# Kernel optimization log

Hardware: AMD Instinct MI355X
Metric: run time of the kernel (lower is better)

Reference implementation:

```python
import jax, jax.numpy as jnp
import numpy as np

GROUPS = 4
SF = 2   # scale_factor
K = 3    # filter_k

def conv1x1(x, w, b):
    return jnp.einsum('bchw,oc->bohw', x, w) + b[None, :, None, None]

def grid_sample(img, grid):
    # img: (N,C,H,W); grid: (N,Hg,Wg,2) xy in [-1,1]; bilinear, border padding, align_corners=False
    N, C, H, W = img.shape
    ix = jnp.clip(((grid[..., 0] + 1.0) * W - 1.0) * 0.5, 0.0, W - 1.0)
    iy = jnp.clip(((grid[..., 1] + 1.0) * H - 1.0) * 0.5, 0.0, H - 1.0)
    x0 = jnp.floor(ix); y0 = jnp.floor(iy)
    wx = (ix - x0)[..., None]; wy = (iy - y0)[..., None]
    x0i = x0.astype(jnp.int32); y0i = y0.astype(jnp.int32)
    x1i = jnp.minimum(x0i + 1, W - 1); y1i = jnp.minimum(y0i + 1, H - 1)
    bidx = jnp.arange(N)[:, None, None]
    v00 = img[bidx, :, y0i, x0i]; v01 = img[bidx, :, y0i, x1i]
    v10 = img[bidx, :, y1i, x0i]; v11 = img[bidx, :, y1i, x1i]   # (N,Hg,Wg,C)
    out = (v00 * (1 - wx) * (1 - wy) + v01 * wx * (1 - wy)
           + v10 * (1 - wx) * wy + v11 * wx * wy)
    return jnp.transpose(out, (0, 3, 1, 2))

def def_sample(x, off):
    b, c, h, w = x.shape
    g = GROUPS
    off = off.reshape(b * g, SF, SF, 2, h, w).transpose(0, 4, 1, 5, 2, 3)
    hd, wd = SF * h, SF * w
    off = off.reshape(b * g, hd, wd, 2)
    gy, gx = jnp.meshgrid(jnp.arange(hd, dtype=x.dtype) + 0.5,
                          jnp.arange(wd, dtype=x.dtype) + 0.5, indexing='ij')
    base = jnp.stack([gx, gy], axis=-1)[None]
    grid = 2.0 * (base + off) / jnp.array([wd, hd], dtype=x.dtype) - 1.0
    return grid_sample(x.reshape(b * g, c // g, h, w), grid).reshape(b, c, hd, wd)

def dyn_filter(x, compress, kw, kb):
    b, c, h, w = x.shape
    kern = jax.nn.softmax(conv1x1(compress, kw, kb), axis=1)  # (b,K*K,h,w)
    p = K // 2
    xp = jnp.pad(x, ((0, 0), (0, 0), (p, p), (p, p)))
    patches = jnp.stack([xp[:, :, dy:dy + h, dx:dx + w]
                         for dy in range(K) for dx in range(K)], axis=2)  # (b,c,K*K,h,w)
    return jnp.einsum('bkhw,bckhw->bchw', kern, patches)

def trim_op(x, toff):
    b, c, h, w = x.shape
    g = GROUPS
    off = toff.reshape(b, g, 2, h, w).transpose(0, 1, 3, 4, 2)  # (b,g,h,w,2) xy
    gy, gx = jnp.meshgrid(jnp.arange(h, dtype=x.dtype) + 0.5,
                          jnp.arange(w, dtype=x.dtype) + 0.5, indexing='ij')
    base = jnp.stack([gx, gy], axis=-1)[None, None]
    grid = (2.0 * (base + off) / jnp.array([w, h], dtype=x.dtype) - 1.0).reshape(b * g, h, w, 2)
    return grid_sample(x.reshape(b * g, c // g, h, w), grid).reshape(b, c, h, w)

def setup_inputs():
    key = jax.random.key(0)
    ks = jax.random.split(key, 13)
    C = 256
    oc = GROUPS * SF * SF * 2  # 32
    f = jnp.float32
    return {
        "x": jax.random.normal(ks[0], (4, C, 64, 64), f),
        "def_off_w": jax.random.normal(ks[1], (oc, C), f) * 0.001,
        "def_off_b": jnp.zeros((oc,), f),
        "def_ast_w": jax.random.normal(ks[2], (oc, C), f) * 0.01,
        "def_ast_b": jnp.zeros((oc,), f),
        "comp_w": jax.random.normal(ks[3], (64, C), f) * (1.0 / np.sqrt(C).astype(np.float32)),
        "comp_b": jnp.zeros((64,), f),
        "filt_w": jax.random.normal(ks[4], (K * K, 64), f) * 0.001,
        "filt_b": jnp.zeros((K * K,), f),
        "trim_w": jax.random.normal(ks[5], (GROUPS * 2, 64), f) * 0.001,
        "trim_b": jnp.zeros((GROUPS * 2,), f),
        "trim_ast_w": jax.random.normal(ks[6], (GROUPS * 2, 64), f) * 0.01,
        "trim_ast_b": jnp.zeros((GROUPS * 2,), f),
    }

def reference(x, def_off_w, def_off_b, def_ast_w, def_ast_b, comp_w, comp_b,
              filt_w, filt_b, trim_w, trim_b, trim_ast_w, trim_ast_b):
    off = conv1x1(x, def_off_w, def_off_b) * jax.nn.sigmoid(conv1x1(x, def_ast_w, def_ast_b))
    x_up = def_sample(x, off)                              # (b,c,2h,2w)
    comp = conv1x1(x_up, comp_w, comp_b)                   # (b,64,2h,2w)
    x_filt = dyn_filter(x_up, comp, filt_w, filt_b)
    toff = conv1x1(comp, trim_w, trim_b) * jax.nn.sigmoid(conv1x1(comp, trim_ast_w, trim_ast_b))
    return trim_op(x_filt, toff)
```

## Files before the change

kernel.cpp:

```cpp
#include <hip/hip_runtime.h>
#include <hip/hip_bf16.h>
#include <string.h>

typedef __hip_bfloat16 bf16;
typedef __attribute__((ext_vector_type(8))) short short8;
typedef __attribute__((ext_vector_type(4))) short short4v;
typedef __attribute__((ext_vector_type(4))) float f32x4;

__device__ __forceinline__ float b2f(bf16 v) { return __bfloat162float(v); }
__device__ __forceinline__ bf16  f2b(float v) { return __float2bfloat16(v); }
__device__ __forceinline__ float s2f(short s) {
    return __uint_as_float(((unsigned)(unsigned short)s) << 16);
}
__device__ __forceinline__ short f2s(float v) {
    bf16 t = f2b(v); short s; __builtin_memcpy(&s, &t, 2); return s;
}

#define CC 256
#define HWD 16384

__global__ __launch_bounds__(256) void k0_xpose(const float* __restrict__ x,
        bf16* __restrict__ xpm)
{
    __shared__ short tile[64][258];
    int b = blockIdx.x >> 6;
    int p0 = (blockIdx.x & 63) << 6;
    int lp = threadIdx.x & 63;
    int c0 = threadIdx.x >> 6;
    const float* xb = x + ((size_t)b << 20);
    for (int k = 0; k < 64; ++k) {
        int c = c0 * 64 + k;
        tile[lp][c] = f2s(xb[((size_t)c << 12) + p0 + lp]);
    }
    __syncthreads();
    int lc = threadIdx.x & 63;
    int s = threadIdx.x >> 6;
    short* ob = (short*)xpm + ((size_t)(b * 4096 + p0) << 8) + s * 64 + lc;
    for (int r = 0; r < 64; ++r)
        ob[(size_t)r << 8] = tile[r][s * 64 + lc];
}

__global__ __launch_bounds__(256) void k1_off(const bf16* __restrict__ xpm,
        const float* __restrict__ w_off, const float* __restrict__ b_off,
        const float* __restrict__ w_ast, const float* __restrict__ b_ast,
        float* __restrict__ offpm)
{
    const int b = blockIdx.x >> 6;
    const int p0 = (blockIdx.x & 63) << 6;
    const int lane = threadIdx.x & 63;
    const int n = lane & 15, quad = lane >> 4;
    const int jb = (threadIdx.x >> 6) << 4;
    const int j = jb + n, oc = j >> 1, kind = j & 1;

    short8 bfrag[8];
    const float* wrow = (kind ? w_ast : w_off) + oc * 256 + quad * 8;
#pragma unroll
    for (int kc = 0; kc < 8; ++kc) {
        float4 lo = *(const float4*)(wrow + kc * 32);
        float4 hi = *(const float4*)(wrow + kc * 32 + 4);
        short8 f;
        f[0] = f2s(lo.x); f[1] = f2s(lo.y); f[2] = f2s(lo.z); f[3] = f2s(lo.w);
        f[4] = f2s(hi.x); f[5] = f2s(hi.y); f[6] = f2s(hi.z); f[7] = f2s(hi.w);
        bfrag[kc] = f;
    }
    float bias = kind ? b_ast[oc] : b_off[oc];

    const short* abase = (const short*)xpm + ((size_t)(b * 4096) << 8);
    float* obase = offpm + ((size_t)(b * 4096) << 5);

#pragma unroll
    for (int mt = 0; mt < 4; mt += 2) {
        f32x4 acc0 = {0.f, 0.f, 0.f, 0.f};
        f32x4 acc1 = {0.f, 0.f, 0.f, 0.f};
        const short8* ar0 = (const short8*)(abase + (((size_t)(p0 + mt * 16 + n)) << 8) + quad * 8);
        const short8* ar1 = (const short8*)(abase + (((size_t)(p0 + mt * 16 + 16 + n)) << 8) + quad * 8);
#pragma unroll
        for (int kc = 0; kc < 8; ++kc) {
            short8 a0 = ar0[kc * 4];
            short8 a1 = ar1[kc * 4];
            acc0 = __builtin_amdgcn_mfma_f32_16x16x32_bf16(a0, bfrag[kc], acc0, 0, 0, 0);
            acc1 = __builtin_amdgcn_mfma_f32_16x16x32_bf16(a1, bfrag[kc], acc1, 0, 0, 0);
        }
#pragma unroll
        for (int r = 0; r < 4; ++r) {
            float v0 = acc0[r] + bias;
            float v1 = acc1[r] + bias;
            float p0v = __shfl_xor(v0, 1, 64);
            float p1v = __shfl_xor(v1, 1, 64);
            if (!(n & 1)) {
                int px = p0 + mt * 16 + quad * 4 + r;
                obase[((size_t)px << 5) + oc] = v0 * (1.f / (1.f + expf(-p0v)));
                obase[((size_t)(px + 16) << 5) + oc] = v1 * (1.f / (1.f + expf(-p1v)));
            }
        }
    }
}

__global__ __launch_bounds__(256) void k2_defsample(const bf16* __restrict__ xpm,
        const float* __restrict__ offpm, bf16* __restrict__ xup)
{
    int p = blockIdx.x * 4 + (threadIdx.x >> 6);
    int lane = threadIdx.x & 63;
    int b = p >> 14, hw = p & 16383;
    int hy = hw >> 7, wx = hw & 127;
    int h = hy >> 1, w = wx >> 1;
    int g = lane >> 4;
    int och = (g << 3) + ((hy & 1) << 2) + ((wx & 1) << 1);
    const float* orow = offpm + ((size_t)(b * 4096 + (h << 6) + w) << 5);
    float ox = orow[och], oy = orow[och + 1];
    float ix = (wx + 0.5f + ox) * 0.5f - 0.5f;
    float iy = (hy + 0.5f + oy) * 0.5f - 0.5f;
    ix = fminf(fmaxf(ix, 0.f), 63.f);
    iy = fminf(fmaxf(iy, 0.f), 63.f);
    float x0f = floorf(ix), y0f = floorf(iy);
    float fx = ix - x0f, fy = iy - y0f;
    int x0 = (int)x0f, y0 = (int)y0f;
    int x1 = min(x0 + 1, 63), y1 = min(y0 + 1, 63);
    float w00 = (1.f - fx) * (1.f - fy), w01 = fx * (1.f - fy);
    float w10 = (1.f - fx) * fy,        w11 = fx * fy;
    const short* xb = (const short*)xpm + ((size_t)b << 20);
    int e = lane * 4;
    short4v v00 = *(const short4v*)(xb + (((size_t)(y0 << 6) + x0) << 8) + e);
    short4v v01 = *(const short4v*)(xb + (((size_t)(y0 << 6) + x1) << 8) + e);
    short4v v10 = *(const short4v*)(xb + (((size_t)(y1 << 6) + x0) << 8) + e);
    short4v v11 = *(const short4v*)(xb + (((size_t)(y1 << 6) + x1) << 8) + e);
    short4v pk;
#pragma unroll
    for (int j = 0; j < 4; ++j) {
        float v = w00 * s2f(v00[j]) + w01 * s2f(v01[j])
                + w10 * s2f(v10[j]) + w11 * s2f(v11[j]);
        pk[j] = f2s(v);
    }
    *(short4v*)((short*)xup + (((size_t)(b * HWD + hw)) << 8) + e) = pk;
}

__global__ __launch_bounds__(256) void k3_fused(const bf16* __restrict__ xup,
        const float* __restrict__ cw, const float* __restrict__ cb,
        const float* __restrict__ fw_g, const float* __restrict__ fb,
        const float* __restrict__ tw, const float* __restrict__ tb,
        const float* __restrict__ taw, const float* __restrict__ tab,
        bf16* __restrict__ kern, float* __restrict__ toff)
{
    __shared__ float smc[64][65];
    __shared__ __align__(16) float fwS[64 * 12];
    __shared__ __align__(16) float swS[64 * 16];
    for (int i = threadIdx.x; i < 64 * 12; i += 256) {
        int c = i / 12, k = i % 12;
        fwS[i] = (k < 9) ? fw_g[k * 64 + c] : 0.f;
    }
    for (int i = threadIdx.x; i < 64 * 16; i += 256) {
        int c = i >> 4, jj = i & 15;
        int oc = jj >> 1, kind = jj & 1;
        swS[i] = kind ? taw[oc * 64 + c] : tw[oc * 64 + c];
    }

    const int b = blockIdx.x >> 8;
    const int hw0 = (blockIdx.x & 255) << 6;
    const int lane = threadIdx.x & 63;
    const int n = lane & 15, quad = lane >> 4;
    const int ocb = (threadIdx.x >> 6) << 4;

    short8 bfrag[8];
    const float* wrow = cw + (ocb + n) * 256 + quad * 8;
#pragma unroll
    for (int kc = 0; kc < 8; ++kc) {
        float4 lo = *(const float4*)(wrow + kc * 32);
        float4 hi = *(const float4*)(wrow + kc * 32 + 4);
        short8 f;
        f[0] = f2s(lo.x); f[1] = f2s(lo.y); f[2] = f2s(lo.z); f[3] = f2s(lo.w);
        f[4] = f2s(hi.x); f[5] = f2s(hi.y); f[6] = f2s(hi.z); f[7] = f2s(hi.w);
        bfrag[kc] = f;
    }
    float bias = cb[ocb + n];

    const short* abase = (const short*)xup + ((size_t)(b * HWD) << 8);

#pragma unroll
    for (int mt = 0; mt < 4; mt += 2) {
        f32x4 acc0 = {0.f, 0.f, 0.f, 0.f};
        f32x4 acc1 = {0.f, 0.f, 0.f, 0.f};
        const short8* ar0 = (const short8*)(abase + (((size_t)(hw0 + mt * 16 + n)) << 8) + quad * 8);
        const short8* ar1 = (const short8*)(abase + (((size_t)(hw0 + mt * 16 + 16 + n)) << 8) + quad * 8);
#pragma unroll
        for (int kc = 0; kc < 8; ++kc) {
            short8 a0 = ar0[kc * 4];
            short8 a1 = ar1[kc * 4];
            acc0 = __builtin_amdgcn_mfma_f32_16x16x32_bf16(a0, bfrag[kc], acc0, 0, 0, 0);
            acc1 = __builtin_amdgcn_mfma_f32_16x16x32_bf16(a1, bfrag[kc], acc1, 0, 0, 0);
        }
#pragma unroll
        for (int r = 0; r < 4; ++r) {
            smc[mt * 16 + quad * 4 + r][ocb + n] = acc0[r] + bias;
            smc[mt * 16 + 16 + quad * 4 + r][ocb + n] = acc1[r] + bias;
        }
    }
    __syncthreads();

    const int px = threadIdx.x & 63;
    const int q = threadIdx.x >> 6;
    const int hw = hw0 + px;
    if (q == 0) {
        float a[9];
#pragma unroll
        for (int k = 0; k < 9; ++k) a[k] = fb[k];
        for (int c = 0; c < 64; ++c) {
            float v = smc[px][c];
            const float4* wr = reinterpret_cast<const float4*>(&fwS[c * 12]);
            float4 w0 = wr[0], w1 = wr[1];
            float w8 = fwS[c * 12 + 8];
            a[0] += v * w0.x; a[1] += v * w0.y; a[2] += v * w0.z; a[3] += v * w0.w;
            a[4] += v * w1.x; a[5] += v * w1.y; a[6] += v * w1.z; a[7] += v * w1.w;
            a[8] += v * w8;
        }
        float mx = a[0];
#pragma unroll
        for (int k = 1; k < 9; ++k) mx = fmaxf(mx, a[k]);
        float s = 0.f;
#pragma unroll
        for (int k = 0; k < 9; ++k) { a[k] = expf(a[k] - mx); s += a[k]; }
        float inv = 1.f / s;
        short* kr = (short*)kern + ((size_t)(b * HWD + hw) << 4);
        short8 pk;
#pragma unroll
        for (int k = 0; k < 8; ++k) pk[k] = f2s(a[k] * inv);
        *(short8*)kr = pk;
        kr[8] = f2s(a[8] * inv);
    } else {
        const int oc0 = (q == 3) ? 6 : (q - 1) * 3;
        const int noc = (q == 3) ? 2 : 3;
        float o[3], aa[3];
        for (int i = 0; i < noc; ++i) { o[i] = tb[oc0 + i]; aa[i] = tab[oc0 + i]; }
        for (int c = 0; c < 64; ++c) {
            float v = smc[px][c];
            const float* wr = &swS[c << 4];
#pragma unroll 3
            for (int i = 0; i < noc; ++i) {
                o[i]  += v * wr[2 * (oc0 + i)];
                aa[i] += v * wr[2 * (oc0 + i) + 1];
            }
        }
        for (int i = 0; i < noc; ++i)
            toff[((size_t)(b * 8 + oc0 + i) << 14) + hw] =
                o[i] * (1.f / (1.f + expf(-aa[i])));
    }
}

__global__ __launch_bounds__(256) void k4b_apply(const bf16* __restrict__ xup,
        const bf16* __restrict__ kern, bf16* __restrict__ xfilt)
{
    int t = blockIdx.x * 256 + threadIdx.x;
    int chunk = t & 31;
    int hw = (t >> 5) & 16383;
    int b = t >> 19;
    int h = hw >> 7, w = hw & 127;

    const short* kr = (const short*)kern + ((size_t)(b * HWD + hw) << 4);
    short8 k8 = *(const short8*)kr;
    float wk[9];
#pragma unroll
    for (int k = 0; k < 8; ++k) wk[k] = s2f(k8[k]);
    wk[8] = s2f(kr[8]);

    float ymask[3] = { h > 0 ? 1.f : 0.f, 1.f, h < 127 ? 1.f : 0.f };
    float xmask[3] = { w > 0 ? 1.f : 0.f, 1.f, w < 127 ? 1.f : 0.f };
    int hy[3] = { (max(h - 1, 0)) << 7, h << 7, (min(h + 1, 127)) << 7 };
    int wx[3] = { max(w - 1, 0), w, min(w + 1, 127) };

    const short* xb = (const short*)xup + ((size_t)(b * HWD) << 8) + chunk * 8;
    float sum[8];
#pragma unroll
    for (int j = 0; j < 8; ++j) sum[j] = 0.f;
#pragma unroll
    for (int dy = 0; dy < 3; ++dy) {
#pragma unroll
        for (int dx = 0; dx < 3; ++dx) {
            float wgt = wk[dy * 3 + dx] * ymask[dy] * xmask[dx];
            short8 v = *(const short8*)(xb + ((size_t)(hy[dy] + wx[dx]) << 8));
#pragma unroll
            for (int j = 0; j < 8; ++j) sum[j] += wgt * s2f(v[j]);
        }
    }
    short8 pk;
#pragma unroll
    for (int j = 0; j < 8; ++j) pk[j] = f2s(sum[j]);
    *(short8*)((short*)xfilt + ((size_t)(b * HWD + hw) << 8) + chunk * 8) = pk;
}

__global__ __launch_bounds__(256) void k6_trim(const bf16* __restrict__ xfilt,
        const float* __restrict__ toff, float* __restrict__ out)
{
    __shared__ float sm[32][260];
    int b = blockIdx.x >> 9;
    int hw0 = (blockIdx.x & 511) << 5;
    int wave = threadIdx.x >> 6, lane = threadIdx.x & 63;
    int e = lane * 4;
    int g = lane >> 4;
    const short* xb = (const short*)xfilt + ((size_t)(b * HWD) << 8);
    const float* tfx = toff + ((size_t)(b * 8 + 2 * g)     << 14);
    const float* tfy = toff + ((size_t)(b * 8 + 2 * g + 1) << 14);

    for (int i = 0; i < 8; ++i) {
        int pp = wave * 8 + i;
        int hw = hw0 + pp;
        int h = hw >> 7, w = hw & 127;
        float ox = tfx[hw], oy = tfy[hw];
        float ix = fminf(fmaxf(w + ox, 0.f), 127.f);
        float iy = fminf(fmaxf(h + oy, 0.f), 127.f);
        float x0f = floorf(ix), y0f = floorf(iy);
        float fx = ix - x0f, fy = iy - y0f;
        int x0 = (int)x0f, y0 = (int)y0f;
        int x1 = min(x0 + 1, 127), y1 = min(y0 + 1, 127);
        float w00 = (1.f - fx) * (1.f - fy), w01 = fx * (1.f - fy);
        float w10 = (1.f - fx) * fy,        w11 = fx * fy;
        short4v v00 = *(const short4v*)(xb + (((size_t)(y0 << 7) + x0) << 8) + e);
        short4v v01 = *(const short4v*)(xb + (((size_t)(y0 << 7) + x1) << 8) + e);
        short4v v10 = *(const short4v*)(xb + (((size_t)(y1 << 7) + x0) << 8) + e);
        short4v v11 = *(const short4v*)(xb + (((size_t)(y1 << 7) + x1) << 8) + e);
#pragma unroll
        for (int j = 0; j < 4; ++j) {
            sm[pp][e + j] = w00 * s2f(v00[j]) + w01 * s2f(v01[j])
                          + w10 * s2f(v10[j]) + w11 * s2f(v11[j]);
        }
    }
    __syncthreads();
    int lp = threadIdx.x & 31;
    int c0 = (threadIdx.x >> 5) << 5;
    float* ob = out + (((size_t)b << 8) << 14) + hw0 + lp;
#pragma unroll 8
    for (int k = 0; k < 32; ++k) {
        int c = c0 + k;
        ob[(size_t)c << 14] = sm[lp][c];
    }
}

extern "C" void kernel_launch(void* const* d_in, const int* in_sizes, int n_in,
                              void* d_out, int out_size, void* d_ws, size_t ws_size,
                              hipStream_t stream)
{
    const float* x       = (const float*)d_in[0];
    const float* w_off   = (const float*)d_in[1];
    const float* b_off   = (const float*)d_in[2];
    const float* w_ast   = (const float*)d_in[3];
    const float* b_ast   = (const float*)d_in[4];
    const float* comp_w  = (const float*)d_in[5];
    const float* comp_b  = (const float*)d_in[6];
    const float* filt_w  = (const float*)d_in[7];
    const float* filt_b  = (const float*)d_in[8];
    const float* trim_w  = (const float*)d_in[9];
    const float* trim_b  = (const float*)d_in[10];
    const float* trim_aw = (const float*)d_in[11];
    const float* trim_ab = (const float*)d_in[12];
    float* out = (float*)d_out;

    char* ws = (char*)d_ws;
    float* offpm = (float*)(ws);
    bf16*  kern  = (bf16*) (ws);
    bf16*  xup   = (bf16*) (ws + (2ull << 20));
    bf16*  xpm   = (bf16*) (ws + (34ull << 20));
    bf16*  xfilt = (bf16*) (ws + (50ull << 20));
    float* toff  = (float*)(ws + (82ull << 20));

    hipLaunchKernelGGL(k0_xpose,    dim3(256),   dim3(256), 0, stream,
                       x, xpm);
    hipLaunchKernelGGL(k1_off,      dim3(256),   dim3(256), 0, stream,
                       xpm, w_off, b_off, w_ast, b_ast, offpm);
    hipLaunchKernelGGL(k2_defsample,dim3(16384), dim3(256), 0, stream,
                       xpm, offpm, xup);
    hipLaunchKernelGGL(k3_fused,    dim3(1024),  dim3(256), 0, stream,
                       xup, comp_w, comp_b, filt_w, filt_b,
                       trim_w, trim_b, trim_aw, trim_ab, kern, toff);
    hipLaunchKernelGGL(k4b_apply,   dim3(8192),  dim3(256), 0, stream,
                       xup, kern, xfilt);
    hipLaunchKernelGGL(k6_trim,     dim3(2048),  dim3(256), 0, stream,
                       xfilt, toff, out);
}
```

Baseline: 190.9 us.

## Fuse transpose with offset conv and deformable sampling with compress conv

Merges the transpose kernel into the offset conv kernel so the transposed tile stays in swizzled shared memory and feeds the MFMA directly. It also merges deformable sampling into the compress-conv kernel, so the upsampled tile is built in LDS and used for the GEMM without being read back from global memory. The xup buffer is still written for the later filter kernel, and kern moves to its own workspace region because it no longer aliases offpm. Two launches and one global re-read are removed, at the cost of larger shared-memory use and lower occupancy in the fused kernels.

```diff
diff --git a/kernel.cpp b/kernel.cpp
--- a/kernel.cpp
+++ b/kernel.cpp
@@ -19,39 +19,20 @@
 #define CC 256
 #define HWD 16384
 
-__global__ __launch_bounds__(256) void k0_xpose(const float* __restrict__ x,
-        bf16* __restrict__ xpm)
-{
-    __shared__ short tile[64][258];
-    int b = blockIdx.x >> 6;
-    int p0 = (blockIdx.x & 63) << 6;
-    int lp = threadIdx.x & 63;
-    int c0 = threadIdx.x >> 6;
-    const float* xb = x + ((size_t)b << 20);
-    for (int k = 0; k < 64; ++k) {
-        int c = c0 * 64 + k;
-        tile[lp][c] = f2s(xb[((size_t)c << 12) + p0 + lp]);
-    }
-    __syncthreads();
-    int lc = threadIdx.x & 63;
-    int s = threadIdx.x >> 6;
-    short* ob = (short*)xpm + ((size_t)(b * 4096 + p0) << 8) + s * 64 + lc;
-    for (int r = 0; r < 64; ++r)
-        ob[(size_t)r << 8] = tile[r][s * 64 + lc];
-}
-
-__global__ __launch_bounds__(256) void k1_off(const bf16* __restrict__ xpm,
+__global__ __launch_bounds__(256) void k01_xpose_off(const float* __restrict__ x,
         const float* __restrict__ w_off, const float* __restrict__ b_off,
         const float* __restrict__ w_ast, const float* __restrict__ b_ast,
-        float* __restrict__ offpm)
-{
+        bf16* __restrict__ xpm, float* __restrict__ offpm)
+{
+    __shared__ __align__(16) short tileS[64 * 256];
     const int b = blockIdx.x >> 6;
     const int p0 = (blockIdx.x & 63) << 6;
     const int lane = threadIdx.x & 63;
+    const int wave = threadIdx.x >> 6;
     const int n = lane & 15, quad = lane >> 4;
-    const int jb = (threadIdx.x >> 6) << 4;
+
+    const int jb = wave << 4;
     const int j = jb + n, oc = j >> 1, kind = j & 1;
-
     short8 bfrag[8];
     const float* wrow = (kind ? w_ast : w_off) + oc * 256 + quad * 8;
 #pragma unroll
@@ -65,19 +46,44 @@
     }
     float bias = kind ? b_ast[oc] : b_off[oc];
 
-    const short* abase = (const short*)xpm + ((size_t)(b * 4096) << 8);
-    float* obase = offpm + ((size_t)(b * 4096) << 5);
-
+    {
+        const float* xb = x + ((size_t)b << 20);
+        const int lp = lane;
+        const int c0 = wave;
+#pragma unroll
+        for (int gg = 0; gg < 8; ++gg) {
+            int cbase = (c0 << 6) + (gg << 3);
+            short8 pk;
+#pragma unroll
+            for (int jj = 0; jj < 8; ++jj)
+                pk[jj] = f2s(xb[((size_t)(cbase + jj) << 12) + p0 + lp]);
+            int slot = (cbase >> 3) ^ (lp & 7);
+            *(short8*)&tileS[(lp << 8) + (slot << 3)] = pk;
+        }
+    }
+    __syncthreads();
+
+    {
+        short* ob = (short*)xpm + ((size_t)((b << 12) + p0) << 8);
+#pragma unroll
+        for (int rr = 0; rr < 16; ++rr) {
+            int r = (wave << 4) + rr;
+            short4v v = *(const short4v*)&tileS[(r << 8)
+                        + ((((lane >> 1) ^ (r & 7)) << 3) | ((lane & 1) << 2))];
+            *(short4v*)(ob + ((size_t)r << 8) + (lane << 2)) = v;
+        }
+    }
+
+    float* obase = offpm + ((size_t)(b << 12) << 5);
 #pragma unroll
     for (int mt = 0; mt < 4; mt += 2) {
         f32x4 acc0 = {0.f, 0.f, 0.f, 0.f};
         f32x4 acc1 = {0.f, 0.f, 0.f, 0.f};
-        const short8* ar0 = (const short8*)(abase + (((size_t)(p0 + mt * 16 + n)) << 8) + quad * 8);
-        const short8* ar1 = (const short8*)(abase + (((size_t)(p0 + mt * 16 + 16 + n)) << 8) + quad * 8);
 #pragma unroll
         for (int kc = 0; kc < 8; ++kc) {
-            short8 a0 = ar0[kc * 4];
-            short8 a1 = ar1[kc * 4];
+            int slot = (((kc << 2) + quad) ^ (n & 7)) << 3;
+            short8 a0 = *(const short8*)&tileS[((mt * 16 + n) << 8) + slot];
+            short8 a1 = *(const short8*)&tileS[((mt * 16 + 16 + n) << 8) + slot];
             acc0 = __builtin_amdgcn_mfma_f32_16x16x32_bf16(a0, bfrag[kc], acc0, 0, 0, 0);
             acc1 = __builtin_amdgcn_mfma_f32_16x16x32_bf16(a1, bfrag[kc], acc1, 0, 0, 0);
         }
@@ -96,52 +102,15 @@
     }
 }
 
-__global__ __launch_bounds__(256) void k2_defsample(const bf16* __restrict__ xpm,
-        const float* __restrict__ offpm, bf16* __restrict__ xup)
-{
-    int p = blockIdx.x * 4 + (threadIdx.x >> 6);
-    int lane = threadIdx.x & 63;
-    int b = p >> 14, hw = p & 16383;
-    int hy = hw >> 7, wx = hw & 127;
-    int h = hy >> 1, w = wx >> 1;
-    int g = lane >> 4;
-    int och = (g << 3) + ((hy & 1) << 2) + ((wx & 1) << 1);
-    const float* orow = offpm + ((size_t)(b * 4096 + (h << 6) + w) << 5);
-    float ox = orow[och], oy = orow[och + 1];
-    float ix = (wx + 0.5f + ox) * 0.5f - 0.5f;
-    float iy = (hy + 0.5f + oy) * 0.5f - 0.5f;
-    ix = fminf(fmaxf(ix, 0.f), 63.f);
-    iy = fminf(fmaxf(iy, 0.f), 63.f);
-    float x0f = floorf(ix), y0f = floorf(iy);
-    float fx = ix - x0f, fy = iy - y0f;
-    int x0 = (int)x0f, y0 = (int)y0f;
-    int x1 = min(x0 + 1, 63), y1 = min(y0 + 1, 63);
-    float w00 = (1.f - fx) * (1.f - fy), w01 = fx * (1.f - fy);
-    float w10 = (1.f - fx) * fy,        w11 = fx * fy;
-    const short* xb = (const short*)xpm + ((size_t)b << 20);
-    int e = lane * 4;
-    short4v v00 = *(const short4v*)(xb + (((size_t)(y0 << 6) + x0) << 8) + e);
-    short4v v01 = *(const short4v*)(xb + (((size_t)(y0 << 6) + x1) << 8) + e);
-    short4v v10 = *(const short4v*)(xb + (((size_t)(y1 << 6) + x0) << 8) + e);
-    short4v v11 = *(const short4v*)(xb + (((size_t)(y1 << 6) + x1) << 8) + e);
-    short4v pk;
-#pragma unroll
-    for (int j = 0; j < 4; ++j) {
-        float v = w00 * s2f(v00[j]) + w01 * s2f(v01[j])
-                + w10 * s2f(v10[j]) + w11 * s2f(v11[j]);
-        pk[j] = f2s(v);
-    }
-    *(short4v*)((short*)xup + (((size_t)(b * HWD + hw)) << 8) + e) = pk;
-}
-
-__global__ __launch_bounds__(256) void k3_fused(const bf16* __restrict__ xup,
+__global__ __launch_bounds__(256) void k23_defsample_comp(
+        const bf16* __restrict__ xpm, const float* __restrict__ offpm,
         const float* __restrict__ cw, const float* __restrict__ cb,
         const float* __restrict__ fw_g, const float* __restrict__ fb,
         const float* __restrict__ tw, const float* __restrict__ tb,
         const float* __restrict__ taw, const float* __restrict__ tab,
-        bf16* __restrict__ kern, float* __restrict__ toff)
-{
-    __shared__ float smc[64][65];
+        bf16* __restrict__ xup, bf16* __restrict__ kern, float* __restrict__ toff)
+{
+    __shared__ __align__(16) short xupS[64 * 256];
     __shared__ __align__(16) float fwS[64 * 12];
     __shared__ __align__(16) float swS[64 * 16];
     for (int i = threadIdx.x; i < 64 * 12; i += 256) {
@@ -157,8 +126,9 @@
     const int b = blockIdx.x >> 8;
     const int hw0 = (blockIdx.x & 255) << 6;
     const int lane = threadIdx.x & 63;
+    const int wave = threadIdx.x >> 6;
     const int n = lane & 15, quad = lane >> 4;
-    const int ocb = (threadIdx.x >> 6) << 4;
+    const int ocb = wave << 4;
 
     short8 bfrag[8];
     const float* wrow = cw + (ocb + n) * 256 + quad * 8;
@@ -173,26 +143,70 @@
     }
     float bias = cb[ocb + n];
 
-    const short* abase = (const short*)xup + ((size_t)(b * HWD) << 8);
-
-#pragma unroll
-    for (int mt = 0; mt < 4; mt += 2) {
-        f32x4 acc0 = {0.f, 0.f, 0.f, 0.f};
-        f32x4 acc1 = {0.f, 0.f, 0.f, 0.f};
-        const short8* ar0 = (const short8*)(abase + (((size_t)(hw0 + mt * 16 + n)) << 8) + quad * 8);
-        const short8* ar1 = (const short8*)(abase + (((size_t)(hw0 + mt * 16 + 16 + n)) << 8) + quad * 8);
-#pragma unroll
-        for (int kc = 0; kc < 8; ++kc) {
-            short8 a0 = ar0[kc * 4];
-            short8 a1 = ar1[kc * 4];
-            acc0 = __builtin_amdgcn_mfma_f32_16x16x32_bf16(a0, bfrag[kc], acc0, 0, 0, 0);
-            acc1 = __builtin_amdgcn_mfma_f32_16x16x32_bf16(a1, bfrag[kc], acc1, 0, 0, 0);
-        }
-#pragma unroll
-        for (int r = 0; r < 4; ++r) {
-            smc[mt * 16 + quad * 4 + r][ocb + n] = acc0[r] + bias;
-            smc[mt * 16 + 16 + quad * 4 + r][ocb + n] = acc1[r] + bias;
-        }
+    {
+        const short* xsrc = (const short*)xpm + ((size_t)b << 20);
+        const int e = lane << 2;
+        const int g = lane >> 4;
+#pragma unroll 2
+        for (int i = 0; i < 16; ++i) {
+            int pp = (wave << 4) + i;
+            int hw = hw0 + pp;
+            int hy = hw >> 7, wx = hw & 127;
+            int h = hy >> 1, w = wx >> 1;
+            int och = (g << 3) + ((hy & 1) << 2) + ((wx & 1) << 1);
+            const float* orow = offpm + ((size_t)((b << 12) + (h << 6) + w) << 5);
+            float ox = orow[och], oy = orow[och + 1];
+            float ix = (wx + 0.5f + ox) * 0.5f - 0.5f;
+            float iy = (hy + 0.5f + oy) * 0.5f - 0.5f;
+            ix = fminf(fmaxf(ix, 0.f), 63.f);
+            iy = fminf(fmaxf(iy, 0.f), 63.f);
+            float x0f = floorf(ix), y0f = floorf(iy);
+            float fx = ix - x0f, fy = iy - y0f;
+            int x0 = (int)x0f, y0 = (int)y0f;
+            int x1 = min(x0 + 1, 63), y1 = min(y0 + 1, 63);
+            float w00 = (1.f - fx) * (1.f - fy), w01 = fx * (1.f - fy);
+            float w10 = (1.f - fx) * fy,        w11 = fx * fy;
+            short4v v00 = *(const short4v*)(xsrc + (((size_t)(y0 << 6) + x0) << 8) + e);
+            short4v v01 = *(const short4v*)(xsrc + (((size_t)(y0 << 6) + x1) << 8) + e);
+            short4v v10 = *(const short4v*)(xsrc + (((size_t)(y1 << 6) + x0) << 8) + e);
+            short4v v11 = *(const short4v*)(xsrc + (((size_t)(y1 << 6) + x1) << 8) + e);
+            short4v pk;
+#pragma unroll
+            for (int jj = 0; jj < 4; ++jj) {
+                float v = w00 * s2f(v00[jj]) + w01 * s2f(v01[jj])
+                        + w10 * s2f(v10[jj]) + w11 * s2f(v11[jj]);
+                pk[jj] = f2s(v);
+            }
+            *(short4v*)((short*)xup + (((size_t)((b << 14) + hw)) << 8) + e) = pk;
+            *(short4v*)&xupS[(pp << 8)
+                    + ((((e >> 3) ^ (pp & 7)) << 3) | (e & 4))] = pk;
+        }
+    }
+    __syncthreads();
+
+    f32x4 accA0 = {0.f,0.f,0.f,0.f}, accA1 = {0.f,0.f,0.f,0.f};
+    f32x4 accB0 = {0.f,0.f,0.f,0.f}, accB1 = {0.f,0.f,0.f,0.f};
+#pragma unroll
+    for (int kc = 0; kc < 8; ++kc) {
+        int slot = (((kc << 2) + quad) ^ (n & 7)) << 3;
+        short8 a0 = *(const short8*)&xupS[((     n) << 8) + slot];
+        short8 a1 = *(const short8*)&xupS[((16 + n) << 8) + slot];
+        short8 a2 = *(const short8*)&xupS[((32 + n) << 8) + slot];
+        short8 a3 = *(const short8*)&xupS[((48 + n) << 8) + slot];
+        accA0 = __builtin_amdgcn_mfma_f32_16x16x32_bf16(a0, bfrag[kc], accA0, 0, 0, 0);
+        accA1 = __builtin_amdgcn_mfma_f32_16x16x32_bf16(a1, bfrag[kc], accA1, 0, 0, 0);
+        accB0 = __builtin_amdgcn_mfma_f32_16x16x32_bf16(a2, bfrag[kc], accB0, 0, 0, 0);
+        accB1 = __builtin_amdgcn_mfma_f32_16x16x32_bf16(a3, bfrag[kc], accB1, 0, 0, 0);
+    }
+    __syncthreads();
+
+    float (*smc)[65] = (float (*)[65])xupS;
+#pragma unroll
+    for (int r = 0; r < 4; ++r) {
+        smc[     quad * 4 + r][ocb + n] = accA0[r] + bias;
+        smc[16 + quad * 4 + r][ocb + n] = accA1[r] + bias;
+        smc[32 + quad * 4 + r][ocb + n] = accB0[r] + bias;
+        smc[48 + quad * 4 + r][ocb + n] = accB1[r] + bias;
     }
     __syncthreads();
 
@@ -219,7 +233,7 @@
 #pragma unroll
         for (int k = 0; k < 9; ++k) { a[k] = expf(a[k] - mx); s += a[k]; }
         float inv = 1.f / s;
-        short* kr = (short*)kern + ((size_t)(b * HWD + hw) << 4);
+        short* kr = (short*)kern + ((size_t)((b << 14) + hw) << 4);
         short8 pk;
 #pragma unroll
         for (int k = 0; k < 8; ++k) pk[k] = f2s(a[k] * inv);
@@ -240,7 +254,7 @@
             }
         }
         for (int i = 0; i < noc; ++i)
-            toff[((size_t)(b * 8 + oc0 + i) << 14) + hw] =
+            toff[((size_t)((b << 3) + oc0 + i) << 14) + hw] =
                 o[i] * (1.f / (1.f + expf(-aa[i])));
     }
 }
@@ -354,21 +368,17 @@
 
     char* ws = (char*)d_ws;
     float* offpm = (float*)(ws);
-    bf16*  kern  = (bf16*) (ws);
     bf16*  xup   = (bf16*) (ws + (2ull << 20));
     bf16*  xpm   = (bf16*) (ws + (34ull << 20));
     bf16*  xfilt = (bf16*) (ws + (50ull << 20));
     float* toff  = (float*)(ws + (82ull << 20));
-
-    hipLaunchKernelGGL(k0_xpose,    dim3(256),   dim3(256), 0, stream,
-                       x, xpm);
-    hipLaunchKernelGGL(k1_off,      dim3(256),   dim3(256), 0, stream,
-                       xpm, w_off, b_off, w_ast, b_ast, offpm);
-    hipLaunchKernelGGL(k2_defsample,dim3(16384), dim3(256), 0, stream,
-                       xpm, offpm, xup);
-    hipLaunchKernelGGL(k3_fused,    dim3(1024),  dim3(256), 0, stream,
-                       xup, comp_w, comp_b, filt_w, filt_b,
-                       trim_w, trim_b, trim_aw, trim_ab, kern, toff);
+    bf16*  kern  = (bf16*) (ws + (84ull << 20));
+
+    hipLaunchKernelGGL(k01_xpose_off, dim3(256),  dim3(256), 0, stream,
+                       x, w_off, b_off, w_ast, b_ast, xpm, offpm);
+    hipLaunchKernelGGL(k23_defsample_comp, dim3(1024), dim3(256), 0, stream,
+                       xpm, offpm, comp_w, comp_b, filt_w, filt_b,
+                       trim_w, trim_b, trim_aw, trim_ab, xup, kern, toff);
     hipLaunchKernelGGL(k4b_apply,   dim3(8192),  dim3(256), 0, stream,
                        xup, kern, xfilt);
     hipLaunchKernelGGL(k6_trim,     dim3(2048),  dim3(256), 0, stream,
```

Measured after the change: 171.7 us. 10.1% less time.
